# Kernel tuning notes

Hardware: AMD Instinct MI355X
Metric: run time of the kernel (lower is better)

Reference implementation:

```python
import jax, jax.numpy as jnp
import numpy as np
import math

B, CIN, COUT, K, G, SD, H = 8, 512, 512, 3, 16, 512, 32
EPS = 1e-8


def _blur_kernel():
    k = jnp.array([1., 3., 3., 1.], dtype=jnp.float32)
    k = k[None, :] * k[:, None]
    k = k / k.sum()
    return k * 4.0  # upsample_factor ** 2


def setup_inputs() -> dict:
    key = jax.random.key(0)
    ks = jax.random.split(key, 10)
    return {
        "x": jax.random.normal(ks[0], (B, CIN, H, H), jnp.float32),
        "co": jax.random.uniform(ks[1], (1, CIN, CIN), jnp.float32),
        "style": jax.random.normal(ks[2], (B, 2 * SD), jnp.float32),
        "noise": jax.random.normal(ks[3], (B, 1, 2 * H, 2 * H), jnp.float32),
        "W": jax.random.normal(ks[4], (1, COUT, CIN, K, K), jnp.float32),
        "mb_w": jax.random.normal(ks[5], (G, SD), jnp.float32),
        "mb_b": jnp.ones((G,), jnp.float32),
        "mod_w": jax.random.normal(ks[6], (CIN, SD), jnp.float32),
        "mod_b": jnp.ones((CIN,), jnp.float32),
        "cluster": jax.random.normal(ks[7], (G, CIN), jnp.float32),
        "gate": -jnp.ones((1,), jnp.float32),
        "tmpr": -2.0 * jnp.ones((1,), jnp.float32),
        "noise_weight": jnp.zeros((1,), jnp.float32),
        "flr_bias": jnp.zeros((COUT,), jnp.float32),
    }


def _l2norm(x, axis):
    n = jnp.linalg.norm(x, axis=axis, keepdims=True)
    return x / jnp.maximum(n, 1e-12)


def reference(x, co, style, noise, W, mb_w, mb_b, mod_w, mod_b,
              cluster, gate, tmpr, noise_weight, flr_bias):
    scale = 1.0 / math.sqrt(CIN * K * K)   # GroupModulatedConv2d.scale
    lin_scale = 1.0 / math.sqrt(SD)        # EqualLinear scale (lr_mul=1)

    t = jax.nn.sigmoid(tmpr) * 5.0
    g = jax.nn.sigmoid(gate)
    S = jax.nn.sigmoid((co - g) * 50.0)                    # (1,Cin,Cin)
    cl = jax.nn.softmax(t * cluster, axis=0)               # (G,Cin)
    loss1 = jnp.sum((cl.T @ cl - jax.lax.stop_gradient(S)) ** 2)
    loss2 = jnp.sum((jnp.float32(CIN * CIN / G) - jnp.sum(S)) ** 2)
    grouped = jax.lax.stop_gradient(jnp.round(jax.nn.softmax(cl * 500.0, axis=0))) + 1e-6

    s1, s2 = style[:, :SD], style[:, SD:]
    style_base = (s1 @ (mb_w * lin_scale).T + mb_b)[:, :, None]   # (B,G,1)
    st = (s2 @ (mod_w * lin_scale).T + mod_b)[:, None, :]         # (B,1,Cin)
    tmp = _l2norm(grouped[None] * st, axis=2)                     # (B,G,Cin)
    st = jnp.sum(tmp * style_base, axis=1)                        # (B,Cin)

    w = scale * W * st[:, None, :, None, None]                    # (B,Cout,Cin,K,K)
    demod = jax.lax.rsqrt(jnp.sum(w * w, axis=(2, 3, 4)) + EPS)   # (B,Cout)
    w = w * demod[:, :, None, None, None]

    # conv_transpose2d(stride=2, pad=0, groups=B) == per-sample conv with
    # lhs_dilation=2, padding=K-1, spatially-flipped kernel.
    wf = w[:, :, :, ::-1, ::-1]

    def per_sample(xi, wi):  # xi (Cin,h,w), wi (Cout,Cin,K,K)
        return jax.lax.conv_general_dilated(
            xi[None], wi, window_strides=(1, 1),
            padding=((K - 1, K - 1), (K - 1, K - 1)), lhs_dilation=(2, 2),
            dimension_numbers=('NCHW', 'OIHW', 'NCHW'))[0]

    out = jax.vmap(per_sample)(x, wf)                             # (B,Cout,65,65)

    # Blur: upfirdn2d, pad=(1,1), depthwise 4x4 symmetric FIR kernel.
    bk = _blur_kernel()
    kdw = jnp.broadcast_to(bk[None, None], (COUT, 1, 4, 4))
    out = jax.lax.conv_general_dilated(
        out, kdw, (1, 1), ((1, 1), (1, 1)), feature_group_count=COUT,
        dimension_numbers=('NCHW', 'OIHW', 'NCHW'))                # (B,Cout,64,64)

    # Correlation of base weights (detached, fed to next layer as `co`).
    wflat = W.reshape(COUT, -1)
    wn = _l2norm(wflat, axis=1)
    co_out = jax.lax.stop_gradient((wn @ wn.T)[None])              # (1,Cout,Cout)

    # NoiseInjection + FusedLeakyReLU
    out = out + noise_weight * noise
    out = jax.nn.leaky_relu(out + flr_bias[None, :, None, None], 0.2) * math.sqrt(2.0)
    return out, co_out, loss1, loss2
```

## Files before the change

### kernel.cpp

```cpp
#include <hip/hip_runtime.h>
#include <hip/hip_bf16.h>

#define NB 8
#define LIN_SCALE 0.044194173824159216f
#define SCALE 0.014731391274719736f

typedef __attribute__((ext_vector_type(8))) short short8;
typedef __attribute__((ext_vector_type(4))) float floatx4;

static constexpr size_t O_XS   = 0;
static constexpr size_t O_OUT1 = 9469952;
static constexpr size_t O_WRT  = 44081152;
static constexpr size_t O_WB   = 48799744;
static constexpr size_t O_PG   = 53518336;
static constexpr size_t O_WSQ  = 61906944;
static constexpr size_t O_CL   = 62955520;
static constexpr size_t O_GR   = O_CL + 32768;
static constexpr size_t O_SB   = O_GR + 32768;
static constexpr size_t O_ST0  = O_SB + 1024;
static constexpr size_t O_STS  = O_ST0 + 16384;
static constexpr size_t O_ST2  = O_STS + 16384;
static constexpr size_t O_WNI  = O_ST2 + 16384;
static constexpr size_t O_DM   = O_WNI + 2048;
static constexpr size_t O_ACC  = O_DM + 16384;

static constexpr size_t OUT_CO = 16777216;
static constexpr size_t OUT_L  = 17039360;

__device__ const int c_ylim[4] = {33,33,32,32};
__device__ const int c_xlim[4] = {33,32,33,32};
__device__ const int c_ntap[4] = {4,2,2,1};
__device__ const int c_tap0[4] = {0,4,6,8};
__device__ const int c_nmb[4]  = {69,66,66,64};
__device__ const int c_cnt[4]  = {276,264,264,256};
__device__ const int c_dy[9] = {-1,-1,0,0, -1,0, 0,0, 0};
__device__ const int c_dx[9] = {-1,0,-1,0, 0,0, -1,0, 0};
__device__ const int c_ky[9] = {2,2,0,0, 2,0, 1,1, 1};
__device__ const int c_kx[9] = {2,0,2,0, 1,1, 2,0, 1};
__device__ const long c_poff[4] = {0, 4460544, 8785920, 13111296};

__device__ __forceinline__ float wave_red(float v) {
#pragma unroll
  for (int s = 32; s > 0; s >>= 1) v += __shfl_down(v, s);
  return v;
}

__device__ __forceinline__ void gl_lds16(const void* g, void* l) {
  __builtin_amdgcn_global_load_lds((const __attribute__((address_space(1))) void*)g,
                                   (__attribute__((address_space(3))) void*)l, 16, 0, 0);
}

__device__ __forceinline__ unsigned short bf16b(float f) {
  union { __hip_bfloat16 h; unsigned short u; } cv;
  cv.h = __float2bfloat16(f);
  return cv.u;
}

__device__ __forceinline__ float bfu(unsigned short u) {
  union { float f; unsigned u32; } c; c.u32 = ((unsigned)u) << 16; return c.f;
}

__device__ __forceinline__ int xcd_chunk(int lb, int cnt) {
  const int q = cnt >> 3, r = cnt & 7;
  const int c = lb & 7, i = lb >> 3;
  return (c < r) ? c*(q+1) + i : r*(q+1) + (c - r)*q + i;
}

__global__ __launch_bounds__(256) void k_big1(const float* __restrict__ W,
    float* __restrict__ wsq, float* __restrict__ wni,
    __hip_bfloat16* __restrict__ wrt,
    const float* __restrict__ style, const float* __restrict__ mod_w,
    const float* __restrict__ mod_b, float* __restrict__ st0,
    const float* __restrict__ co, const float* __restrict__ gate,
    const float* __restrict__ cluster, const float* __restrict__ tmpr,
    const float* __restrict__ mb_w, const float* __restrict__ mb_b,
    float* __restrict__ gr, float* __restrict__ sb,
    float* __restrict__ pacc, __hip_bfloat16* __restrict__ xs) {
  __shared__ float sh[8192];
  __shared__ float extra[8];
  const int bid = blockIdx.x, tid = threadIdx.x;
  const int lane = tid & 63, wv = tid >> 6;
  if (bid < 512) {
    const int o = bid;
    for (int j = tid; j < 4608; j += 256) sh[j] = W[(size_t)o*4608 + j];
    __syncthreads();
    float tot = 0.f;
#pragma unroll
    for (int half = 0; half < 2; half++) {
      const int i = tid + half*256;
      float s = 0.f;
#pragma unroll
      for (int k = 0; k < 9; k++) { float w = sh[i*9 + k]; s = fmaf(w, w, s); }
      wsq[o*512 + i] = s; tot += s;
#pragma unroll
      for (int tp = 0; tp < 9; tp++)
        wrt[((size_t)tp*512 + o)*512 + i] = __float2bfloat16(sh[i*9 + c_ky[tp]*3 + c_kx[tp]]);
    }
    tot = wave_red(tot);
    if (lane == 0) extra[wv] = tot;
    __syncthreads();
    if (tid == 0) wni[o] = 1.f / fmaxf(sqrtf(extra[0]+extra[1]+extra[2]+extra[3]), 1e-12f);
  } else if (bid < 576) {
    const int b = (bid - 512) >> 3, oc = (bid - 512) & 7;
    sh[tid] = style[b*1024 + 512 + tid];
    sh[tid + 256] = style[b*1024 + 768 + tid];
    __syncthreads();
#pragma unroll
    for (int rr = 0; rr < 16; rr++) {
      const int c = oc*64 + wv*16 + rr;
      const float* mw = mod_w + (size_t)c*512;
      float acc = 0.f;
#pragma unroll
      for (int it = 0; it < 8; it++) acc = fmaf(mw[lane + 64*it], sh[lane + 64*it], acc);
      acc = wave_red(acc);
      if (lane == 0) st0[b*512 + c] = acc*LIN_SCALE + mod_b[c];
    }
  } else if (bid < 1088) {
    const int i = bid - 576;
    const float tt = 5.f / (1.f + expf(-tmpr[0]));
    const float gg = 1.f / (1.f + expf(-gate[0]));
    for (int j = tid; j < 512; j += 256) {
      float v[16]; float m = -1e30f;
#pragma unroll
      for (int g = 0; g < 16; g++) { v[g] = tt * cluster[g*512 + j]; m = fmaxf(m, v[g]); }
      float s = 0.f;
#pragma unroll
      for (int g = 0; g < 16; g++) { v[g] = expf(v[g] - m); s += v[g]; }
      float inv = 1.f / s;
#pragma unroll
      for (int g = 0; g < 16; g++) sh[g*512 + j] = v[g] * inv;
    }
    __syncthreads();
    float cli[16];
#pragma unroll
    for (int k = 0; k < 16; k++) cli[k] = sh[k*512 + i];
    float p1 = 0.f, p2 = 0.f;
    for (int j = tid; j < 512; j += 256) {
      float d = 0.f;
#pragma unroll
      for (int k = 0; k < 16; k++) d = fmaf(cli[k], sh[k*512 + j], d);
      float S = 1.f / (1.f + expf(-50.f*(co[i*512 + j] - gg)));
      float e = d - S;
      p1 = fmaf(e, e, p1); p2 += S;
    }
    p1 = wave_red(p1); p2 = wave_red(p2);
    if (lane == 0) { extra[wv] = p1; extra[4 + wv] = p2; }
    __syncthreads();
    if (tid == 0)  pacc[i]       = extra[0]+extra[1]+extra[2]+extra[3];
    if (tid == 64) pacc[512 + i] = extra[4]+extra[5]+extra[6]+extra[7];
  } else if (bid == 1088) {
    const float tt = 5.f / (1.f + expf(-tmpr[0]));
#pragma unroll
    for (int h = 0; h < 2; h++) {
      const int c = tid + h*256;
      float v[16]; float m = -1e30f;
#pragma unroll
      for (int g = 0; g < 16; g++) { v[g] = tt * cluster[g*512 + c]; m = fmaxf(m, v[g]); }
      float s = 0.f;
#pragma unroll
      for (int g = 0; g < 16; g++) { v[g] = expf(v[g] - m); s += v[g]; }
      float inv = 1.f / s;
      float clv[16]; float m2 = -1e30f;
#pragma unroll
      for (int g = 0; g < 16; g++) { clv[g] = v[g]*inv; m2 = fmaxf(m2, 500.f*clv[g]); }
      float s2 = 0.f; float e2[16];
#pragma unroll
      for (int g = 0; g < 16; g++) { e2[g] = expf(500.f*clv[g] - m2); s2 += e2[g]; }
      float i2 = 1.f / s2;
#pragma unroll
      for (int g = 0; g < 16; g++) gr[g*512 + c] = rintf(e2[g]*i2) + 1e-6f;
    }
    for (int task = wv; task < 128; task += 4) {
      int b = task >> 4, g = task & 15;
      const float* s1 = style + b*1024;
      const float* mw = mb_w + g*512;
      float acc = 0.f;
#pragma unroll
      for (int it = 0; it < 8; it++) acc = fmaf(s1[lane + 64*it], mw[lane + 64*it], acc);
      acc = wave_red(acc);
      if (lane == 0) sb[b*16 + g] = acc*LIN_SCALE + mb_b[g];
    }
  } else {
    const int id0 = (bid - 1089)*256 + tid;
    const float4 z = make_float4(0.f, 0.f, 0.f, 0.f);
    float4* xq = (float4*)xs;
#pragma unroll
    for (int it = 0; it < 22; ++it) {
      const int id = id0 + it*3072;
      const int c = id & 63;
      const int pb = id >> 6;
      const int b = pb / 132;
      const int pix = pb - b*132;
      int y, xx;
      if (pix < 34)       { y = 0;        xx = pix; }
      else if (pix < 68)  { y = 33;       xx = pix - 34; }
      else if (pix < 100) { y = pix - 67; xx = 0; }
      else                { y = pix - 99; xx = 33; }
      xq[((size_t)(b*34 + y)*34 + xx)*64 + c] = z;
    }
  }
}

__global__ __launch_bounds__(256) void k_big2(const float* __restrict__ st0,
    const float* __restrict__ gr, const float* __restrict__ sb,
    const float* __restrict__ wsq, float* __restrict__ dm,
    const float* __restrict__ x, __hip_bfloat16* __restrict__ xs,
    const float* __restrict__ pacc, float* __restrict__ out_tail) {
  __shared__ float L[64*65];
  __shared__ float red[16][4];
  __shared__ float inv[16];
  __shared__ float sbb[16];
  const int tid = threadIdx.x;
  const int lane = tid & 63, wv = tid >> 6;

  if (blockIdx.x == 1088) {
    float a = pacc[tid] + pacc[tid + 256];
    float b2 = pacc[512 + tid] + pacc[768 + tid];
    a = wave_red(a); b2 = wave_red(b2);
    if (lane == 0) { red[0][wv] = a; red[1][wv] = b2; }
    __syncthreads();
    if (tid == 0) {
      float p1 = red[0][0]+red[0][1]+red[0][2]+red[0][3];
      float p2 = red[1][0]+red[1][1]+red[1][2]+red[1][3];
      out_tail[0] = p1;
      float d = 16384.f - p2;
      out_tail[1] = d*d;
    }
    return;
  }

  const int b = (blockIdx.x < 64) ? (blockIdx.x >> 3) : ((blockIdx.x - 64) >> 7);
  float s0 = st0[b*512 + tid], s1 = st0[b*512 + 256 + tid];
  float g0[16], g1[16];
#pragma unroll
  for (int g = 0; g < 16; g++) { g0[g] = gr[g*512 + tid]; g1[g] = gr[g*512 + 256 + tid]; }
#pragma unroll
  for (int g = 0; g < 16; g++) {
    float a = g0[g]*s0, c = g1[g]*s1;
    float p = wave_red(a*a + c*c);
    if (lane == 0) red[g][wv] = p;
  }
  if (tid < 16) sbb[tid] = sb[b*16 + tid];
  __syncthreads();
  if (tid < 16) {
    float ttn = red[tid][0] + red[tid][1] + red[tid][2] + red[tid][3];
    inv[tid] = 1.f / fmaxf(sqrtf(ttn), 1e-12f);
  }
  __syncthreads();
  float f0 = 0.f, f1 = 0.f;
#pragma unroll
  for (int g = 0; g < 16; g++) {
    float w = inv[g]*sbb[g];
    f0 = fmaf(g0[g], w, f0); f1 = fmaf(g1[g], w, f1);
  }
  const float sn0 = s0*f0, sn1 = s1*f1;

  if (blockIdx.x < 64) {
    const int oc = blockIdx.x & 7;
    L[tid] = sn0*sn0;
    L[tid + 256] = sn1*sn1;
    __syncthreads();
#pragma unroll
    for (int rr = 0; rr < 16; rr++) {
      const int o = oc*64 + wv*16 + rr;
      const float* wp = wsq + (size_t)o*512;
      float acc = 0.f;
#pragma unroll
      for (int it = 0; it < 8; it++) acc = fmaf(wp[lane + 64*it], L[lane + 64*it], acc);
      acc = wave_red(acc);
      if (lane == 0) dm[b*512 + o] = rsqrtf((1.0f/4608.0f)*acc + 1e-8f);
    }
    return;
  }

  L[tid] = sn0*SCALE;
  L[tid + 256] = sn1*SCALE;
  __syncthreads();
  const int id = blockIdx.x - 64;
  const int p0 = ((id >> 3) & 15) * 64;
  const int i0 = (id & 7) * 64;
  const int iw2 = (tid & 31) * 2, pw = tid >> 5;
  const float sv0 = L[i0 + iw2];
  const float sv1 = L[i0 + iw2 + 1];
  __syncthreads();
  const int cg = (tid & 15) * 4, ir = tid >> 4;
  const float* xp = x + ((size_t)b*512 + i0)*1024 + p0;
  float4 xv[4];
#pragma unroll
  for (int ii = 0; ii < 4; ii++) {
    const int i = ir + 16*ii;
    xv[ii] = *(const float4*)(xp + (size_t)i*1024 + cg);
  }
#pragma unroll
  for (int ii = 0; ii < 4; ii++) {
    const int i = ir + 16*ii;
    L[i*65 + cg + 0] = xv[ii].x;
    L[i*65 + cg + 1] = xv[ii].y;
    L[i*65 + cg + 2] = xv[ii].z;
    L[i*65 + cg + 3] = xv[ii].w;
  }
  __syncthreads();
#pragma unroll
  for (int pp = 0; pp < 8; pp++) {
    const int po = pw + 8*pp;
    const int pix = p0 + po;
    const int y = pix >> 5, xq = pix & 31;
    ushort2 w;
    w.x = bf16b(L[iw2*65 + po] * sv0);
    w.y = bf16b(L[(iw2+1)*65 + po] * sv1);
    *(ushort2*)((unsigned short*)xs + (((size_t)b*34 + (y+1))*34 + (xq+1))*512 + i0 + iw2) = w;
  }
}

__global__ __launch_bounds__(256, 3) void k_mfma(
    const __hip_bfloat16* __restrict__ xs, const __hip_bfloat16* __restrict__ wrt,
    __hip_bfloat16* __restrict__ out1, float* __restrict__ pgram) {
  __shared__ __hip_bfloat16 smem[24576];
  const int fid = blockIdx.x;
  const int tid = threadIdx.x;
  const int lane = tid & 63, wv = tid >> 6;
  const int wm = (wv >> 1) << 6, wn = (wv & 1) << 6;
  const int col16 = lane & 15, quad = lane >> 4;
  const int colp = col16 ^ ((col16 >> 2) & 1);
  const int soff = (quad ^ (col16 & 3)) << 3;

  int aoff[4], boff[4];
#pragma unroll
  for (int t = 0; t < 4; t++) {
    aoff[t] = (wm + t*16 + colp)*32 + soff;
    boff[t] = 4096 + (wn + t*16 + colp)*32 + soff;
  }
  floatx4 acc[4][4];
#pragma unroll
  for (int i = 0; i < 4; i++)
#pragma unroll
    for (int j = 0; j < 4; j++) acc[i][j] = (floatx4){0.f, 0.f, 0.f, 0.f};

  if (fid >= 276 && fid < 324) {
    const int g = xcd_chunk(fid - 276, 48);
    const int ts = g >> 4;
    const int mn = g & 15;
    const int m0 = (mn & 3) * 128, n0 = (mn >> 2) * 128;
    long abase[2], bbase[2]; int ldso[2];
#pragma unroll
    for (int r = 0; r < 2; r++) {
      const int idx = r*256 + tid;
      const int rowp = idx >> 2;
      const int row = rowp ^ ((rowp >> 2) & 1);
      const int kc = (((idx & 3) ^ (row & 3)) << 3);
      abase[r] = ((long)(ts*1536 + m0 + row))*512 + kc;
      bbase[r] = ((long)(ts*1536 + n0 + row))*512 + kc;
      ldso[r] = idx << 3;
    }
#define STAGE_GRAM(s_, lo_) do { \
      const long del_ = ((long)((s_) >> 4) << 18) + (((s_) & 15) << 5); \
      gl_lds16(wrt + (abase[0] + del_), smem + (lo_) + ldso[0]); \
      gl_lds16(wrt + (abase[1] + del_), smem + (lo_) + ldso[1]); \
      gl_lds16(wrt + (bbase[0] + del_), smem + (lo_) + 4096 + ldso[0]); \
      gl_lds16(wrt + (bbase[1] + del_), smem + (lo_) + 4096 + ldso[1]); \
    } while (0)
    STAGE_GRAM(0, 0);
    STAGE_GRAM(1, 8192);
    int loC = 0, loS = 16384;
    for (int s = 0; s < 48; ++s) {
      if (s + 1 < 48) asm volatile("s_waitcnt vmcnt(4)\n\ts_barrier" ::: "memory");
      else            asm volatile("s_waitcnt vmcnt(0)\n\ts_barrier" ::: "memory");
      if (s + 2 < 48) STAGE_GRAM(s + 2, loS);
      short8 af[4], bfr[4];
#pragma unroll
      for (int t = 0; t < 4; t++) {
        af[t]  = *(const short8*)(smem + loC + aoff[t]);
        bfr[t] = *(const short8*)(smem + loC + boff[t]);
      }
#pragma unroll
      for (int i = 0; i < 4; i++)
#pragma unroll
        for (int j = 0; j < 4; j++)
          acc[i][j] = __builtin_amdgcn_mfma_f32_16x16x32_bf16(af[i], bfr[j], acc[i][j], 0, 0, 0);
      loC = (loC == 16384) ? 0 : loC + 8192;
      loS = (loS == 16384) ? 0 : loS + 8192;
    }
    float* pg = pgram + (size_t)ts * 262144;
#pragma unroll
    for (int i = 0; i < 4; i++)
#pragma unroll
      for (int j = 0; j < 4; j++) {
        const int m = m0 + wm + i*16 + (quad << 2);
        const int n = n0 + wn + j*16 + col16;
#pragma unroll
        for (int r = 0; r < 4; r++) pg[(size_t)(m + r)*512 + n] = acc[i][j][r];
      }
    return;
  }

  int cls, lb;
  if (fid < 276)      { cls = 0; lb = fid; }
  else if (fid < 588) { cls = 1; lb = fid - 324; }
  else if (fid < 852) { cls = 2; lb = fid - 588; }
  else                { cls = 3; lb = fid - 852; }
  const int lg = xcd_chunk(lb, c_cnt[cls]);
  const int mb = lg >> 2, nb = lg & 3;
  const int xlim = c_xlim[cls];
  const int npix = c_ylim[cls] * xlim;
  const int M = NB * npix;
  const int m0 = mb * 128, n0 = nb * 128;
  const int t0 = c_tap0[cls];
  const int ntap = c_ntap[cls];

  long abase[2], bbase[2]; int ldso[2];
#pragma unroll
  for (int r = 0; r < 2; r++) {
    const int idx = r*256 + tid;
    const int rowp = idx >> 2;
    const int row = rowp ^ ((rowp >> 2) & 1);
    const int kc = (((idx & 3) ^ (row & 3)) << 3);
    int rm = m0 + row; if (rm >= M) rm = 0;
    const int b = rm / npix; const int rem = rm - b*npix;
    const int yy = rem / xlim; const int xx = rem - yy*xlim;
    abase[r] = ((long)(b*34 + yy + 1)*34 + (xx + 1))*512 + kc;
    bbase[r] = ((long)(t0*512 + n0 + row))*512 + kc;
    ldso[r] = idx << 3;
  }

  const int nst = ntap << 4;
#define STAGE_CONV(s_, lo_) do { \
    const int tap_ = t0 + ((s_) >> 4); \
    const long adel_ = (long)((c_dy[tap_]*34 + c_dx[tap_])*512); \
    const long bdel_ = (long)((s_) >> 4) << 18; \
    const int kk_ = ((s_) & 15) << 5; \
    gl_lds16(xs + (abase[0] + adel_ + kk_), smem + (lo_) + ldso[0]); \
    gl_lds16(xs + (abase[1] + adel_ + kk_), smem + (lo_) + ldso[1]); \
    gl_lds16(wrt + (bbase[0] + bdel_ + kk_), smem + (lo_) + 4096 + ldso[0]); \
    gl_lds16(wrt + (bbase[1] + bdel_ + kk_), smem + (lo_) + 4096 + ldso[1]); \
  } while (0)
  STAGE_CONV(0, 0);
  STAGE_CONV(1, 8192);
  int loC = 0, loS = 16384;
  for (int s = 0; s < nst; ++s) {
    if (s + 1 < nst) asm volatile("s_waitcnt vmcnt(4)\n\ts_barrier" ::: "memory");
    else             asm volatile("s_waitcnt vmcnt(0)\n\ts_barrier" ::: "memory");
    if (s + 2 < nst) STAGE_CONV(s + 2, loS);
    short8 af[4], bfr[4];
#pragma unroll
    for (int t = 0; t < 4; t++) {
      af[t]  = *(const short8*)(smem + loC + aoff[t]);
      bfr[t] = *(const short8*)(smem + loC + boff[t]);
    }
#pragma unroll
    for (int i = 0; i < 4; i++)
#pragma unroll
      for (int j = 0; j < 4; j++)
        acc[i][j] = __builtin_amdgcn_mfma_f32_16x16x32_bf16(af[i], bfr[j], acc[i][j], 0, 0, 0);
    loC = (loC == 16384) ? 0 : loC + 8192;
    loS = (loS == 16384) ? 0 : loS + 8192;
  }

  __syncthreads();
  __hip_bfloat16* plane = out1 + c_poff[cls];
#pragma unroll
  for (int h = 0; h < 2; h++) {
    if ((wv & 1) == h) {
#pragma unroll
      for (int i = 0; i < 4; i++) {
        const int mrow = wm + i*16 + (quad << 2);
#pragma unroll
        for (int j = 0; j < 4; j++) {
          const int ncl = j*16 + col16;
          ushort4 v;
          v.x = bf16b(acc[i][j][0]); v.y = bf16b(acc[i][j][1]);
          v.z = bf16b(acc[i][j][2]); v.w = bf16b(acc[i][j][3]);
          *(ushort4*)(smem + ncl*138 + mrow) = v;
        }
      }
    }
    __syncthreads();
#pragma unroll
    for (int it = 0; it < 4; it++) {
      const int c = it*256 + tid;
      const int ol = c >> 4, ml = (c & 15) << 3;
      const int mg = m0 + ml;
      if (mg < M) {
        const ushort4 v = *(const ushort4*)(smem + ol*138 + ml);
        *(ushort4*)(plane + (long)(n0 + h*64 + ol)*M + mg) = v;
      }
    }
    __syncthreads();
  }
}

__global__ __launch_bounds__(256) void k_blur(const __hip_bfloat16* __restrict__ out1,
    const float* __restrict__ dm, const float* __restrict__ noise,
    const float* __restrict__ nw, const float* __restrict__ fb, float* __restrict__ out,
    const float* __restrict__ pgram, const float* __restrict__ wni,
    float* __restrict__ co_out) {
  if (blockIdx.x < 256) {
    const int i4 = blockIdx.x*256 + threadIdx.x;
    float4 s = make_float4(0.f, 0.f, 0.f, 0.f);
#pragma unroll
    for (int z = 0; z < 3; z++) {
      const float4 v = ((const float4*)(pgram + (size_t)z*262144))[i4];
      s.x += v.x; s.y += v.y; s.z += v.z; s.w += v.w;
    }
    const float wm = wni[i4 >> 7];
    const float4 wn4 = ((const float4*)wni)[i4 & 127];
    float4 o;
    o.x = s.x*wm*wn4.x; o.y = s.y*wm*wn4.y; o.z = s.z*wm*wn4.z; o.w = s.w*wm*wn4.w;
    ((float4*)co_out)[i4] = o;
    return;
  }
  const int bo = blockIdx.x - 256;
  const int b = bo >> 9, o = bo & 511;
  __shared__ unsigned short L[65 * 68];
  __shared__ float Hs[67 * 64];
  const int tid = threadIdx.x;
  const unsigned short* p0 = (const unsigned short*)out1 + 0        + (long)o * 8712 + b * 1089;
  const unsigned short* p1 = (const unsigned short*)out1 + 4460544  + (long)o * 8448 + b * 1056;
  const unsigned short* p2 = (const unsigned short*)out1 + 8785920  + (long)o * 8448 + b * 1056;
  const unsigned short* p3 = (const unsigned short*)out1 + 13111296 + (long)o * 8192 + b * 1024;
  for (int m = tid; m < 65; m += 256) { L[m*68 + 0] = 0; L[m*68 + 66] = 0; }
  if (tid < 64) { Hs[tid] = 0.f; Hs[66*64 + tid] = 0.f; }
  for (int e = tid; e < 1089; e += 256) { int y = e / 33, x = e - 33*y; L[(2*y)*68 + 2*x + 1] = p0[e]; }
  for (int e2 = tid; e2 < 528; e2 += 256) {
    const int e = e2*2; const int y = e >> 5, x = e & 31;
    const ushort2 u = *(const ushort2*)(p1 + e);
    L[(2*y)*68 + 2*x + 2] = u.x; L[(2*y)*68 + 2*x + 4] = u.y;
  }
  for (int e = tid; e < 1056; e += 256) { int y = e / 33, x = e - 33*y; L[(2*y+1)*68 + 2*x + 1] = p2[e]; }
  for (int e2 = tid; e2 < 512; e2 += 256) {
    const int e = e2*2; const int y = e >> 5, x = e & 31;
    const ushort2 u = *(const ushort2*)(p3 + e);
    L[(2*y+1)*68 + 2*x + 2] = u.x; L[(2*y+1)*68 + 2*x + 4] = u.y;
  }
  __syncthreads();
  for (int e = tid; e < 4160; e += 256) {
    const int m = e >> 6, q = e & 63;
    const unsigned short* row = L + m*68 + q;
    Hs[(m+1)*64 + q] = 0.25f * (bfu(row[0]) + bfu(row[3])) + 0.75f * (bfu(row[1]) + bfu(row[2]));
  }
  __syncthreads();
  const float dmv = dm[bo];
  const float nwv = nw[0];
  const float bv = fb[o];
  const int qx = (tid & 15) << 2;
  const int py = tid >> 4;
  float* op = out + ((size_t)bo << 12);
  const float* npl = noise + ((size_t)b << 12);
#pragma unroll
  for (int pp = 0; pp < 4; pp++) {
    const int P = py + (pp << 4);
    const float4 h0 = *(const float4*)(Hs + (P    )*64 + qx);
    const float4 h1 = *(const float4*)(Hs + (P + 1)*64 + qx);
    const float4 h2 = *(const float4*)(Hs + (P + 2)*64 + qx);
    const float4 h3 = *(const float4*)(Hs + (P + 3)*64 + qx);
    const float4 n4 = *(const float4*)(npl + P*64 + qx);
    float4 ov;
    float s;
    s = 0.25f*(h0.x + h3.x) + 0.75f*(h1.x + h2.x);
    ov.x = fmaf(dmv, s, fmaf(nwv, n4.x, bv)); ov.x = (ov.x >= 0.f ? ov.x : 0.2f*ov.x) * 1.4142135623730951f;
    s = 0.25f*(h0.y + h3.y) + 0.75f*(h1.y + h2.y);
    ov.y = fmaf(dmv, s, fmaf(nwv, n4.y, bv)); ov.y = (ov.y >= 0.f ? ov.y : 0.2f*ov.y) * 1.4142135623730951f;
    s = 0.25f*(h0.z + h3.z) + 0.75f*(h1.z + h2.z);
    ov.z = fmaf(dmv, s, fmaf(nwv, n4.z, bv)); ov.z = (ov.z >= 0.f ? ov.z : 0.2f*ov.z) * 1.4142135623730951f;
    s = 0.25f*(h0.w + h3.w) + 0.75f*(h1.w + h2.w);
    ov.w = fmaf(dmv, s, fmaf(nwv, n4.w, bv)); ov.w = (ov.w >= 0.f ? ov.w : 0.2f*ov.w) * 1.4142135623730951f;
    *(float4*)(op + P*64 + qx) = ov;
  }
}

extern "C" void kernel_launch(void* const* d_in, const int* in_sizes, int n_in,
                              void* d_out, int out_size, void* d_ws, size_t ws_size,
                              hipStream_t stream) {
  const float* x       = (const float*)d_in[0];
  const float* co      = (const float*)d_in[1];
  const float* style   = (const float*)d_in[2];
  const float* noise   = (const float*)d_in[3];
  const float* W       = (const float*)d_in[4];
  const float* mb_w    = (const float*)d_in[5];
  const float* mb_b    = (const float*)d_in[6];
  const float* mod_w   = (const float*)d_in[7];
  const float* mod_b   = (const float*)d_in[8];
  const float* cluster = (const float*)d_in[9];
  const float* gate    = (const float*)d_in[10];
  const float* tmpr    = (const float*)d_in[11];
  const float* nw      = (const float*)d_in[12];
  const float* fb      = (const float*)d_in[13];
  float* out = (float*)d_out;
  char* ws = (char*)d_ws;

  __hip_bfloat16* xs   = (__hip_bfloat16*)(ws + O_XS);
  __hip_bfloat16* out1 = (__hip_bfloat16*)(ws + O_OUT1);
  __hip_bfloat16* wrt  = (__hip_bfloat16*)(ws + O_WRT);
  float* pgram = (float*)(ws + O_PG);
  float* wsq = (float*)(ws + O_WSQ);
  float* gr  = (float*)(ws + O_GR);
  float* sb  = (float*)(ws + O_SB);
  float* st0 = (float*)(ws + O_ST0);
  float* wni = (float*)(ws + O_WNI);
  float* dm  = (float*)(ws + O_DM);
  float* pacc = (float*)(ws + O_STS);

  k_big1<<<1101, 256, 0, stream>>>(W, wsq, wni, wrt,
                                   style, mod_w, mod_b, st0, co, gate,
                                   cluster, tmpr, mb_w, mb_b, gr, sb, pacc, xs);
  k_big2<<<1089, 256, 0, stream>>>(st0, gr, sb, wsq, dm, x, xs, pacc, out + OUT_L);
  k_mfma<<<1108, 256, 0, stream>>>(xs, wrt, out1, pgram);
  k_blur<<<4352, 256, 0, stream>>>(out1, dm, noise, nw, fb, out, pgram, wni, out + OUT_CO);
}
```

Measured before the change: 237.5 us.

## Load B operand fragments directly from global into registers, bypassing LDS

The weight (B) operand of the MFMA GEMM loops is no longer staged through shared memory. Each wave now loads its B fragments straight from global memory into double-buffered registers. Only the A operand still goes through LDS, which halves the shared-memory footprint and cuts LDS write/read traffic. The cost is B loads without cross-wave sharing, since two waves read the same B tile, plus more vector registers and a more intricate vmcnt wait scheme that could expose global-load latency.

```diff
diff --git a/kernel.cpp b/kernel.cpp
--- a/kernel.cpp
+++ b/kernel.cpp
@@ -315,7 +315,7 @@
 __global__ __launch_bounds__(256, 3) void k_mfma(
     const __hip_bfloat16* __restrict__ xs, const __hip_bfloat16* __restrict__ wrt,
     __hip_bfloat16* __restrict__ out1, float* __restrict__ pgram) {
-  __shared__ __hip_bfloat16 smem[24576];
+  __shared__ __hip_bfloat16 smem[12288];
   const int fid = blockIdx.x;
   const int tid = threadIdx.x;
   const int lane = tid & 63, wv = tid >> 6;
@@ -324,12 +324,9 @@
   const int colp = col16 ^ ((col16 >> 2) & 1);
   const int soff = (quad ^ (col16 & 3)) << 3;
 
-  int aoff[4], boff[4];
-#pragma unroll
-  for (int t = 0; t < 4; t++) {
-    aoff[t] = (wm + t*16 + colp)*32 + soff;
-    boff[t] = 4096 + (wn + t*16 + colp)*32 + soff;
-  }
+  int aoff[4];
+#pragma unroll
+  for (int t = 0; t < 4; t++) aoff[t] = (wm + t*16 + colp)*32 + soff;
   floatx4 acc[4][4];
 #pragma unroll
   for (int i = 0; i < 4; i++)
@@ -341,7 +338,7 @@
     const int ts = g >> 4;
     const int mn = g & 15;
     const int m0 = (mn & 3) * 128, n0 = (mn >> 2) * 128;
-    long abase[2], bbase[2]; int ldso[2];
+    long abase[2]; int ldso[2];
 #pragma unroll
     for (int r = 0; r < 2; r++) {
       const int idx = r*256 + tid;
@@ -349,36 +346,53 @@
       const int row = rowp ^ ((rowp >> 2) & 1);
       const int kc = (((idx & 3) ^ (row & 3)) << 3);
       abase[r] = ((long)(ts*1536 + m0 + row))*512 + kc;
-      bbase[r] = ((long)(ts*1536 + n0 + row))*512 + kc;
       ldso[r] = idx << 3;
     }
-#define STAGE_GRAM(s_, lo_) do { \
-      const long del_ = ((long)((s_) >> 4) << 18) + (((s_) & 15) << 5); \
-      gl_lds16(wrt + (abase[0] + del_), smem + (lo_) + ldso[0]); \
-      gl_lds16(wrt + (abase[1] + del_), smem + (lo_) + ldso[1]); \
-      gl_lds16(wrt + (bbase[0] + del_), smem + (lo_) + 4096 + ldso[0]); \
-      gl_lds16(wrt + (bbase[1] + del_), smem + (lo_) + 4096 + ldso[1]); \
+    const __hip_bfloat16* bp[4];
+#pragma unroll
+    for (int t = 0; t < 4; t++)
+      bp[t] = wrt + ((size_t)(ts*1536 + n0 + wn + t*16 + col16))*512 + (quad << 3);
+#define GDEL(s_) (((long)((s_) >> 4) << 18) + (((s_) & 15) << 5))
+#define STAGE_GA(s_, lo_) do { \
+      const long d_ = GDEL(s_); \
+      gl_lds16(wrt + (abase[0] + d_), smem + (lo_) + ldso[0]); \
+      gl_lds16(wrt + (abase[1] + d_), smem + (lo_) + ldso[1]); \
     } while (0)
-    STAGE_GRAM(0, 0);
-    STAGE_GRAM(1, 8192);
-    int loC = 0, loS = 16384;
-    for (int s = 0; s < 48; ++s) {
-      if (s + 1 < 48) asm volatile("s_waitcnt vmcnt(4)\n\ts_barrier" ::: "memory");
+#define LOADB(dst_, s_) do { \
+      const long d_ = GDEL(s_); \
+      dst_[0] = *(const short8*)(bp[0] + d_); \
+      dst_[1] = *(const short8*)(bp[1] + d_); \
+      dst_[2] = *(const short8*)(bp[2] + d_); \
+      dst_[3] = *(const short8*)(bp[3] + d_); \
+    } while (0)
+#define MFMA16(b_) do { \
+      short8 af_[4]; \
+      _Pragma("unroll") \
+      for (int t = 0; t < 4; t++) af_[t] = *(const short8*)(smem + loC + aoff[t]); \
+      _Pragma("unroll") \
+      for (int i = 0; i < 4; i++) \
+        _Pragma("unroll") \
+        for (int j = 0; j < 4; j++) \
+          acc[i][j] = __builtin_amdgcn_mfma_f32_16x16x32_bf16(af_[i], b_[j], acc[i][j], 0, 0, 0); \
+    } while (0)
+#define ROT(v_) v_ = (v_ == 8192) ? 0 : v_ + 4096
+    short8 bE[4], bO[4];
+    STAGE_GA(0, 0); LOADB(bE, 0);
+    __builtin_amdgcn_sched_barrier(0);
+    STAGE_GA(1, 4096); LOADB(bO, 1);
+    int loC = 0, loS = 8192;
+    for (int s = 0; s < 48; s += 2) {
+      asm volatile("s_waitcnt vmcnt(6)\n\ts_barrier" ::: "memory");
+      if (s + 2 < 48) STAGE_GA(s + 2, loS);
+      MFMA16(bE);
+      if (s + 2 < 48) LOADB(bE, s + 2);
+      ROT(loC); ROT(loS);
+      if (s + 2 < 48) asm volatile("s_waitcnt vmcnt(6)\n\ts_barrier" ::: "memory");
       else            asm volatile("s_waitcnt vmcnt(0)\n\ts_barrier" ::: "memory");
-      if (s + 2 < 48) STAGE_GRAM(s + 2, loS);
-      short8 af[4], bfr[4];
-#pragma unroll
-      for (int t = 0; t < 4; t++) {
-        af[t]  = *(const short8*)(smem + loC + aoff[t]);
-        bfr[t] = *(const short8*)(smem + loC + boff[t]);
-      }
-#pragma unroll
-      for (int i = 0; i < 4; i++)
-#pragma unroll
-        for (int j = 0; j < 4; j++)
-          acc[i][j] = __builtin_amdgcn_mfma_f32_16x16x32_bf16(af[i], bfr[j], acc[i][j], 0, 0, 0);
-      loC = (loC == 16384) ? 0 : loC + 8192;
-      loS = (loS == 16384) ? 0 : loS + 8192;
+      if (s + 3 < 48) STAGE_GA(s + 3, loS);
+      MFMA16(bO);
+      if (s + 3 < 48) LOADB(bO, s + 3);
+      ROT(loC); ROT(loS);
     }
     float* pg = pgram + (size_t)ts * 262144;
 #pragma unroll
@@ -407,7 +421,7 @@
   const int t0 = c_tap0[cls];
   const int ntap = c_ntap[cls];
 
-  long abase[2], bbase[2]; int ldso[2];
+  long abase[2]; int ldso[2];
 #pragma unroll
   for (int r = 0; r < 2; r++) {
     const int idx = r*256 + tid;
@@ -418,41 +432,39 @@
     const int b = rm / npix; const int rem = rm - b*npix;
     const int yy = rem / xlim; const int xx = rem - yy*xlim;
     abase[r] = ((long)(b*34 + yy + 1)*34 + (xx + 1))*512 + kc;
-    bbase[r] = ((long)(t0*512 + n0 + row))*512 + kc;
     ldso[r] = idx << 3;
   }
+  const __hip_bfloat16* bp[4];
+#pragma unroll
+  for (int t = 0; t < 4; t++)
+    bp[t] = wrt + ((size_t)(t0*512 + n0 + wn + t*16 + col16))*512 + (quad << 3);
 
   const int nst = ntap << 4;
-#define STAGE_CONV(s_, lo_) do { \
+#define STAGE_CA(s_, lo_) do { \
     const int tap_ = t0 + ((s_) >> 4); \
-    const long adel_ = (long)((c_dy[tap_]*34 + c_dx[tap_])*512); \
-    const long bdel_ = (long)((s_) >> 4) << 18; \
-    const int kk_ = ((s_) & 15) << 5; \
-    gl_lds16(xs + (abase[0] + adel_ + kk_), smem + (lo_) + ldso[0]); \
-    gl_lds16(xs + (abase[1] + adel_ + kk_), smem + (lo_) + ldso[1]); \
-    gl_lds16(wrt + (bbase[0] + bdel_ + kk_), smem + (lo_) + 4096 + ldso[0]); \
-    gl_lds16(wrt + (bbase[1] + bdel_ + kk_), smem + (lo_) + 4096 + ldso[1]); \
+    const long d_ = (long)((c_dy[tap_]*34 + c_dx[tap_])*512) + (((s_) & 15) << 5); \
+    gl_lds16(xs + (abase[0] + d_), smem + (lo_) + ldso[0]); \
+    gl_lds16(xs + (abase[1] + d_), smem + (lo_) + ldso[1]); \
   } while (0)
-  STAGE_CONV(0, 0);
-  STAGE_CONV(1, 8192);
-  int loC = 0, loS = 16384;
-  for (int s = 0; s < nst; ++s) {
-    if (s + 1 < nst) asm volatile("s_waitcnt vmcnt(4)\n\ts_barrier" ::: "memory");
-    else             asm volatile("s_waitcnt vmcnt(0)\n\ts_barrier" ::: "memory");
-    if (s + 2 < nst) STAGE_CONV(s + 2, loS);
-    short8 af[4], bfr[4];
-#pragma unroll
-    for (int t = 0; t < 4; t++) {
-      af[t]  = *(const short8*)(smem + loC + aoff[t]);
-      bfr[t] = *(const short8*)(smem + loC + boff[t]);
-    }
-#pragma unroll
-    for (int i = 0; i < 4; i++)
-#pragma unroll
-      for (int j = 0; j < 4; j++)
-        acc[i][j] = __builtin_amdgcn_mfma_f32_16x16x32_bf16(af[i], bfr[j], acc[i][j], 0, 0, 0);
-    loC = (loC == 16384) ? 0 : loC + 8192;
-    loS = (loS == 16384) ? 0 : loS + 8192;
+  {
+    short8 bE[4], bO[4];
+    STAGE_CA(0, 0); LOADB(bE, 0);
+    __builtin_amdgcn_sched_barrier(0);
+    STAGE_CA(1, 4096); LOADB(bO, 1);
+    int loC = 0, loS = 8192;
+    for (int s = 0; s < nst; s += 2) {
+      asm volatile("s_waitcnt vmcnt(6)\n\ts_barrier" ::: "memory");
+      if (s + 2 < nst) STAGE_CA(s + 2, loS);
+      MFMA16(bE);
+      if (s + 2 < nst) LOADB(bE, s + 2);
+      ROT(loC); ROT(loS);
+      if (s + 2 < nst) asm volatile("s_waitcnt vmcnt(6)\n\ts_barrier" ::: "memory");
+      else             asm volatile("s_waitcnt vmcnt(0)\n\ts_barrier" ::: "memory");
+      if (s + 3 < nst) STAGE_CA(s + 3, loS);
+      MFMA16(bO);
+      if (s + 3 < nst) LOADB(bO, s + 3);
+      ROT(loC); ROT(loS);
+    }
   }
 
   __syncthreads();
```

Measured after the change: 284.1 us. 1.2x slower.
